# Performance work log

Measured on AMD Instinct MI355X. Metric: run time of the kernel, lower is better.

The kernel has to match this reference:

```python
import jax, jax.numpy as jnp
import numpy as np

HIDDEN = 50
EPS = 1e-5


def setup_inputs() -> dict:
    key = jax.random.key(0)
    ks = jax.random.split(key, 16)
    N = 1_000_000
    G = 10_000
    xy = jax.random.normal(ks[0], (N, 2), dtype=jnp.float32)
    segment_ids = jnp.sort(jax.random.randint(ks[1], (N,), 0, G, dtype=jnp.int32))

    def lin(k, fan_in, shape):
        b = 1.0 / np.sqrt(fan_in)
        return jax.random.uniform(k, shape, jnp.float32, -b, b)

    w_init = lin(ks[2], 2, (2, HIDDEN))
    b_init = lin(ks[3], 2, (HIDDEN,))
    Ws1 = lin(ks[4], 2 * HIDDEN, (2, 2 * HIDDEN, HIDDEN))
    bs1 = lin(ks[5], 2 * HIDDEN, (2, HIDDEN))
    Ws = lin(ks[6], HIDDEN, (2, 4, HIDDEN, HIDDEN))
    bs = lin(ks[7], HIDDEN, (2, 4, HIDDEN))
    gamma = jnp.ones((2, HIDDEN), jnp.float32)
    beta = jnp.zeros((2, HIDDEN), jnp.float32)
    return {
        'xy': xy, 'segment_ids': segment_ids, 'num_graphs': G,
        'w_init': w_init, 'b_init': b_init,
        'Ws1': Ws1, 'bs1': bs1, 'Ws': Ws, 'bs': bs,
        'gamma': gamma, 'beta': beta,
    }


def reference(xy, segment_ids, num_graphs, w_init, b_init, Ws1, bs1, Ws, bs, gamma, beta):
    # node_init: [N,2] -> [N,50]
    h = xy @ w_init + b_init
    ones = jnp.ones((xy.shape[0],), h.dtype)
    counts = jax.ops.segment_sum(ones, segment_ids, num_segments=num_graphs)
    counts = jnp.maximum(counts, 1.0)[:, None]  # [G,1]
    for i in range(2):
        # dgl.mean_nodes -> per-graph mean; dgl.broadcast_nodes -> gather back
        mean = jax.ops.segment_sum(h, segment_ids, num_segments=num_graphs) / counts
        glob = mean[segment_ids]                       # [N,50]
        x = jnp.concatenate([glob, h], axis=1)         # [N,100]
        x = jax.nn.relu(x @ Ws1[i] + bs1[i])
        for j in range(3):
            x = jax.nn.relu(x @ Ws[i, j] + bs[i, j])
        x = x @ Ws[i, 3] + bs[i, 3]
        # BatchNorm1d (training mode: batch stats, biased variance)
        mu = jnp.mean(x, axis=0)
        var = jnp.mean((x - mu) ** 2, axis=0)
        h = (x - mu) * jax.lax.rsqrt(var + EPS) * gamma[i] + beta[i]
    return h
```

## Files before the change

kernel.cpp:

```cpp
#include <hip/hip_runtime.h>


#define GN 10000
#define H 50
#define EPSV 1e-5f

typedef __attribute__((ext_vector_type(4))) float f32x4;
typedef __attribute__((ext_vector_type(2))) __fp16 fp16x2;
typedef __attribute__((ext_vector_type(4))) _Float16 half4_t;

union H4 { half4_t h; uint2 u; };

static __device__ __forceinline__ f32x4 mfma16(half4_t a, half4_t b, f32x4 c){
#if __has_builtin(__builtin_amdgcn_mfma_f32_16x16x16f16)
  return __builtin_amdgcn_mfma_f32_16x16x16f16(a, b, c, 0, 0, 0);
#else
  asm volatile("v_mfma_f32_16x16x16_f16 %0, %1, %2, %0" : "+v"(c) : "v"(a), "v"(b));
  return c;
#endif
}

static __device__ __forceinline__ void split4(f32x4 v, H4& hh, H4& hl){
  fp16x2 a = __builtin_amdgcn_cvt_pkrtz(v[0], v[1]);
  fp16x2 b = __builtin_amdgcn_cvt_pkrtz(v[2], v[3]);
  hh.u.x = __builtin_bit_cast(unsigned int, a);
  hh.u.y = __builtin_bit_cast(unsigned int, b);
  float r0 = v[0] - (float)a[0];
  float r1 = v[1] - (float)a[1];
  float r2 = v[2] - (float)b[0];
  float r3 = v[3] - (float)b[1];
  fp16x2 c = __builtin_amdgcn_cvt_pkrtz(r0, r1);
  fp16x2 d = __builtin_amdgcn_cvt_pkrtz(r2, r3);
  hl.u.x = __builtin_bit_cast(unsigned int, c);
  hl.u.y = __builtin_bit_cast(unsigned int, d);
}

__global__ void k_start(const int* __restrict__ sid, int N, int* __restrict__ start){
  int g = blockIdx.x*blockDim.x + threadIdx.x;
  if (g > GN) return;
  int lo = 0, hi = N;
  while (lo < hi){ int mid = (lo+hi)>>1; if (sid[mid] < g) lo = mid+1; else hi = mid; }
  start[g] = lo;
}

__global__ void k_gsum_xy(const float2* __restrict__ xy, const int* __restrict__ start,
                          float* __restrict__ gxy){
  int g = blockIdx.x; int l = threadIdx.x;
  int s = start[g], e = start[g+1];
  float sx = 0.f, sy = 0.f;
  for (int n = s + l; n < e; n += 64){ float2 v = xy[n]; sx += v.x; sy += v.y; }
  #pragma unroll
  for (int off = 32; off > 0; off >>= 1){ sx += __shfl_down(sx, off); sy += __shfl_down(sy, off); }
  if (l == 0){ gxy[2*g] = sx; gxy[2*g+1] = sy; }
}

template<int LAYER>
__global__ void k_tgraph(const float* __restrict__ gxy, const float* __restrict__ gsum,
                         const int* __restrict__ start,
                         const float* __restrict__ w_init, const float* __restrict__ b_init,
                         const float* __restrict__ Ws1, const float* __restrict__ bs1,
                         const float* __restrict__ stats, float* __restrict__ tg){
  __shared__ float glob[H];
  int g = blockIdx.x; int j = threadIdx.x;
  int cnt = start[g+1] - start[g]; if (cnt < 1) cnt = 1;
  float inv = 1.f/(float)cnt;
  if (j < H){
    if (LAYER == 0){
      float mx = gxy[2*g]*inv, my = gxy[2*g+1]*inv;
      glob[j] = b_init[j] + mx*w_init[j] + my*w_init[H+j];
    } else {
      glob[j] = gsum[g*H+j]*inv*stats[j] + stats[H+j];
    }
  }
  __syncthreads();
  if (j < H){
    const float* W = Ws1 + LAYER*100*H;
    float acc = bs1[LAYER*H + j];
    #pragma unroll 5
    for (int k = 0; k < H; ++k) acc = fmaf(glob[k], W[k*H + j], acc);
    tg[g*H + j] = acc;
  }
}

__global__ void k_wfrag(const float* __restrict__ Ws1, const float* __restrict__ Ws,
                        const float* __restrict__ bs,
                        uint2* __restrict__ frag, float* __restrict__ pbias){
  int t = blockIdx.x*blockDim.x + threadIdx.x;
  if (t < 20480){
    int lane = t & 63;
    int pl   = (t>>6) & 1;
    int ks   = (t>>7) & 3;
    int Mt   = (t>>9) & 3;
    int rest = t >> 11;
    int m = rest % 5, L = rest / 5;
    const float* W = (m == 0) ? (Ws1 + L*100*H + H*H) : (Ws + (L*4 + (m-1))*H*H);
    int jo = Mt*16 + (lane & 15);
    int kb = ks*16 + ((lane>>4)<<2);
    f32x4 v;
    #pragma unroll
    for (int e = 0; e < 4; ++e){
      int k = kb + e;
      v[e] = (k < H && jo < H) ? W[k*H + jo] : 0.f;
    }
    H4 hh, hl;
    split4(v, hh, hl);
    frag[t] = pl ? hl.u : hh.u;
  } else if (t < 20992){
    int i = t - 20480;
    int j = i & 63;
    int row = i >> 6;
    pbias[i] = (j < H) ? bs[row*H + j] : 0.f;
  }
}

template<int LAYER>
__global__ __launch_bounds__(256, 3)
void k_layer(const float2* __restrict__ xy, const int* __restrict__ sid,
             const float* __restrict__ tg, const uint2* __restrict__ frag,
             const float* __restrict__ pbias,
             const float* __restrict__ w_init, const float* __restrict__ b_init,
             const float* __restrict__ stats,
             float* __restrict__ xio, int N)
{
  const int tid = threadIdx.x;
  const int wv = tid >> 6, l = tid & 63, lg = l >> 4, ll = l & 15;
  const int base = blockIdx.x*128 + wv*32;

  H4 bh[2][4], bl[2][4];
  #pragma unroll
  for (int Nt = 0; Nt < 2; ++Nt){
    int node = base + Nt*16 + ll;
    int nc = node < N ? node : N-1;
    float xv[16];
    if (LAYER == 0){
      float2 p = xy[nc];
      #pragma unroll
      for (int ks = 0; ks < 4; ++ks)
        #pragma unroll
        for (int e = 0; e < 4; ++e){
          int k = ks*16 + lg*4 + e; int kc = k < H ? k : H-1;
          xv[ks*4+e] = b_init[kc] + p.x*w_init[kc] + p.y*w_init[H+kc];
        }
    } else {
      #pragma unroll
      for (int ks = 0; ks < 4; ++ks){
        int k0 = ks*16 + lg*4;
        size_t f0 = (size_t)nc*H + k0;
        size_t fm = (size_t)N*H - 2;
        float2 u0 = *(const float2*)(xio + (f0     < fm ? f0     : fm));
        float2 u1 = *(const float2*)(xio + (f0 + 2 < fm ? f0 + 2 : fm));
        float vv[4] = {u0.x, u0.y, u1.x, u1.y};
        #pragma unroll
        for (int e = 0; e < 4; ++e){
          int kc = (k0+e) < H ? (k0+e) : H-1;
          xv[ks*4+e] = vv[e]*stats[kc] + stats[H+kc];
        }
      }
    }
    #pragma unroll
    for (int ks = 0; ks < 4; ++ks){
      f32x4 v; v[0]=xv[ks*4]; v[1]=xv[ks*4+1]; v[2]=xv[ks*4+2]; v[3]=xv[ks*4+3];
      split4(v, bh[Nt][ks], bl[Nt][ks]);
    }
  }

  f32x4 acc[4][2];
  {
    int n0 = base + ll;       n0 = n0 < N ? n0 : N-1;
    int n1 = base + 16 + ll;  n1 = n1 < N ? n1 : N-1;
    const float* t0 = tg + (size_t)sid[n0]*H;
    const float* t1 = tg + (size_t)sid[n1]*H;
    #pragma unroll
    for (int Mt = 0; Mt < 4; ++Mt)
      #pragma unroll
      for (int r = 0; r < 4; ++r){
        int j = Mt*16 + lg*4 + r; int jc = j < H ? j : H-1;
        acc[Mt][0][r] = t0[jc];
        acc[Mt][1][r] = t1[jc];
      }
  }

  #pragma unroll
  for (int m = 0; m < 5; ++m){
    const uint2* fp = frag + (LAYER*5 + m)*2048;
    #pragma unroll
    for (int Mt = 0; Mt < 4; ++Mt){
      H4 ah[4], al[4];
      #pragma unroll
      for (int ks = 0; ks < 4; ++ks){
        ah[ks].u = fp[Mt*512 + ks*128 + l];
        al[ks].u = fp[Mt*512 + ks*128 + 64 + l];
      }
      #pragma unroll
      for (int Nt = 0; Nt < 2; ++Nt){
        f32x4 c = acc[Mt][Nt];
        #pragma unroll
        for (int ks = 0; ks < 4; ++ks) c = mfma16(ah[ks].h, bh[Nt][ks].h, c);
        #pragma unroll
        for (int ks = 0; ks < 4; ++ks) c = mfma16(al[ks].h, bh[Nt][ks].h, c);
        #pragma unroll
        for (int ks = 0; ks < 4; ++ks) c = mfma16(ah[ks].h, bl[Nt][ks].h, c);
        acc[Mt][Nt] = c;
      }
    }
    if (m < 4){
      #pragma unroll
      for (int Mt = 0; Mt < 4; ++Mt){
        const f32x4 bv = *(const f32x4*)(pbias + (LAYER*4 + m)*64 + Mt*16 + (lg<<2));
        #pragma unroll
        for (int Nt = 0; Nt < 2; ++Nt){
          f32x4 v = acc[Mt][Nt];
          v[0]=fmaxf(v[0],0.f); v[1]=fmaxf(v[1],0.f); v[2]=fmaxf(v[2],0.f); v[3]=fmaxf(v[3],0.f);
          split4(v, bh[Nt][Mt], bl[Nt][Mt]);
          acc[Mt][Nt] = bv;
        }
      }
    }
  }

  #pragma unroll
  for (int Nt = 0; Nt < 2; ++Nt){
    int node = base + Nt*16 + ll;
    if (node < N){
      float* row = xio + (size_t)node*H;
      #pragma unroll
      for (int Mt = 0; Mt < 3; ++Mt){
        int j0 = Mt*16 + (lg<<2);
        *(float2*)(row + j0)     = make_float2(acc[Mt][Nt][0], acc[Mt][Nt][1]);
        *(float2*)(row + j0 + 2) = make_float2(acc[Mt][Nt][2], acc[Mt][Nt][3]);
      }
      if (lg == 0)
        *(float2*)(row + 48) = make_float2(acc[3][Nt][0], acc[3][Nt][1]);
    }
  }
}

__global__ void k_stats(const float* __restrict__ x, const int* __restrict__ start,
                        float* __restrict__ gsum, float* __restrict__ psum,
                        float* __restrict__ psq){
  int g = blockIdx.x; int j = threadIdx.x;
  if (j >= H) return;
  int s = start[g], e = start[g+1];
  float acc = 0.f, q = 0.f;
  for (int n = s; n < e; ++n){ float v = x[n*H + j]; acc += v; q = fmaf(v, v, q); }
  gsum[g*H + j] = acc;
  int slot = g & 63;
  atomicAdd(&psum[slot*H + j], acc);
  atomicAdd(&psq[slot*H + j], q);
}

__global__ void k_finalize(const float* __restrict__ psum, const float* __restrict__ psq,
                           const float* __restrict__ gamma, const float* __restrict__ beta,
                           int layer, float ninv, float* __restrict__ stats){
  int j = threadIdx.x;
  if (j >= H) return;
  float s = 0.f, q = 0.f;
  #pragma unroll 8
  for (int p = 0; p < 64; ++p){ s += psum[p*H + j]; q += psq[p*H + j]; }
  float mu  = s*ninv;
  float var = q*ninv - mu*mu;
  float a = rsqrtf(var + EPSV) * gamma[layer*H + j];
  float c = beta[layer*H + j] - mu*a;
  stats[layer*100 + j]     = a;
  stats[layer*100 + H + j] = c;
}

__global__ void k_bnapply(float* __restrict__ x, const float* __restrict__ stats, int N){
  __shared__ float a[H], c[H];
  if (threadIdx.x < H){ a[threadIdx.x] = stats[100 + threadIdx.x]; c[threadIdx.x] = stats[150 + threadIdx.x]; }
  __syncthreads();
  int base = blockIdx.x * (256*H);
  int total = N*H;
  for (int idx = threadIdx.x; idx < 256*H; idx += 256){
    int i = base + idx;
    if (i < total){
      int j = idx - (idx/H)*H;
      x[i] = x[i]*a[j] + c[j];
    }
  }
}

extern "C" void kernel_launch(void* const* d_in, const int* in_sizes, int n_in,
                              void* d_out, int out_size, void* d_ws, size_t ws_size,
                              hipStream_t stream) {
  const float2* xy     = (const float2*)d_in[0];
  const int*    sid    = (const int*)d_in[1];
  const float*  w_init = (const float*)d_in[3];
  const float*  b_init = (const float*)d_in[4];
  const float*  Ws1    = (const float*)d_in[5];
  const float*  bs1    = (const float*)d_in[6];
  const float*  Ws     = (const float*)d_in[7];
  const float*  bs     = (const float*)d_in[8];
  const float*  gamma  = (const float*)d_in[9];
  const float*  beta   = (const float*)d_in[10];
  float* out = (float*)d_out;
  int N = in_sizes[0] / 2;
  const int G = GN;

  char* ws = (char*)d_ws;
  int*   start = (int*)ws;
  float* gxy   = (float*)(ws + 40064);
  float* tg    = (float*)(ws + 120064);
  float* gsum  = (float*)(ws + 2120064);
  float* psum  = (float*)(ws + 4120064);
  float* psq   = (float*)(ws + 4132864);
  float* stats = (float*)(ws + 4145664);
  uint2* wfrag = (uint2*)(ws + 4147200);
  float* pbias = (float*)(ws + 4311040);

  int nb = (N + 127)/128;

  k_wfrag<<<82, 256, 0, stream>>>(Ws1, Ws, bs, wfrag, pbias);
  k_start<<<(G + 1 + 255)/256, 256, 0, stream>>>(sid, N, start);
  k_gsum_xy<<<G, 64, 0, stream>>>(xy, start, gxy);
  k_tgraph<0><<<G, 64, 0, stream>>>(gxy, gsum, start, w_init, b_init, Ws1, bs1, stats, tg);
  k_layer<0><<<nb, 256, 0, stream>>>(xy, sid, tg, wfrag, pbias, w_init, b_init, stats, out, N);

  (void)hipMemsetAsync(psum, 0, 2*64*H*sizeof(float), stream);
  k_stats<<<G, 64, 0, stream>>>(out, start, gsum, psum, psq);
  k_finalize<<<1, 64, 0, stream>>>(psum, psq, gamma, beta, 0, 1.0f/(float)N, stats);

  k_tgraph<1><<<G, 64, 0, stream>>>(gxy, gsum, start, w_init, b_init, Ws1, bs1, stats, tg);
  k_layer<1><<<nb, 256, 0, stream>>>(xy, sid, tg, wfrag, pbias, w_init, b_init, stats, out, N);

  (void)hipMemsetAsync(psum, 0, 2*64*H*sizeof(float), stream);
  k_stats<<<G, 64, 0, stream>>>(out, start, gsum, psum, psq);
  k_finalize<<<1, 64, 0, stream>>>(psum, psq, gamma, beta, 1, 1.0f/(float)N, stats);

  k_bnapply<<<(N + 255)/256, 256, 0, stream>>>(out, stats, N);
}
```

Measured before the change: 839.5 us.

## Fuse BN statistics into layer kernel and merge setup kernels

Each MFMA layer kernel now reduces per-feature sum and sum-of-squares from its register accumulators and atomically adds them into slot buffers, which removes the separate per-graph stats pass over the 200MB activation. The graph-sum for layer 1 moves into a new kernel that also computes the transformed global term. Weight fragment prep, segment-start search and the psum zeroing are merged into one pre-kernel, and k_finalize re-zeroes the buffers so the memsets go away. Weight fragments are packed as uint4 so the hi and lo halves load together. The cost is atomic traffic from every block and an extra activation read in k_gt1.

```diff
diff --git a/kernel.cpp b/kernel.cpp
--- a/kernel.cpp
+++ b/kernel.cpp
@@ -35,91 +35,75 @@
   hl.u.y = __builtin_bit_cast(unsigned int, d);
 }
 
-__global__ void k_start(const int* __restrict__ sid, int N, int* __restrict__ start){
-  int g = blockIdx.x*blockDim.x + threadIdx.x;
-  if (g > GN) return;
-  int lo = 0, hi = N;
-  while (lo < hi){ int mid = (lo+hi)>>1; if (sid[mid] < g) lo = mid+1; else hi = mid; }
-  start[g] = lo;
-}
-
-__global__ void k_gsum_xy(const float2* __restrict__ xy, const int* __restrict__ start,
-                          float* __restrict__ gxy){
+__global__ void k_pre(const float* __restrict__ Ws1, const float* __restrict__ Ws,
+                      const float* __restrict__ bs, const int* __restrict__ sid, int N,
+                      uint4* __restrict__ frag, float* __restrict__ pbias,
+                      int* __restrict__ start, float* __restrict__ pzero){
+  int t = blockIdx.x*blockDim.x + threadIdx.x;
+  if (t < 10240){
+    int lane = t & 63;
+    int ks   = (t>>6) & 3;
+    int Mt   = (t>>8) & 3;
+    int rest = t >> 10;
+    int m = rest % 5, L = rest / 5;
+    const float* W = (m == 0) ? (Ws1 + L*100*H + H*H) : (Ws + (L*4 + (m-1))*H*H);
+    int jo = Mt*16 + (lane & 15);
+    int kb = ks*16 + ((lane>>4)<<2);
+    f32x4 v;
+    #pragma unroll
+    for (int e = 0; e < 4; ++e){
+      int k = kb + e;
+      v[e] = (k < H && jo < H) ? W[k*H + jo] : 0.f;
+    }
+    H4 hh, hl;
+    split4(v, hh, hl);
+    frag[t] = make_uint4(hh.u.x, hh.u.y, hl.u.x, hl.u.y);
+  } else if (t < 10752){
+    int i = t - 10240;
+    int j = i & 63;
+    int row = i >> 6;
+    pbias[i] = (j < H) ? bs[row*H + j] : 0.f;
+  } else if (t < 20753){
+    int g = t - 10752;
+    int lo = 0, hi = N;
+    while (lo < hi){ int mid = (lo+hi)>>1; if (sid[mid] < g) lo = mid+1; else hi = mid; }
+    start[g] = lo;
+  } else if (t >= 20800 && t < 27200){
+    pzero[t - 20800] = 0.f;
+  }
+}
+
+__global__ void k_ginit0(const float2* __restrict__ xy, const int* __restrict__ start,
+                         const float* __restrict__ w_init, const float* __restrict__ b_init,
+                         const float* __restrict__ Ws1, const float* __restrict__ bs1,
+                         float* __restrict__ tg){
+  __shared__ float glob[H];
   int g = blockIdx.x; int l = threadIdx.x;
   int s = start[g], e = start[g+1];
   float sx = 0.f, sy = 0.f;
   for (int n = s + l; n < e; n += 64){ float2 v = xy[n]; sx += v.x; sy += v.y; }
   #pragma unroll
-  for (int off = 32; off > 0; off >>= 1){ sx += __shfl_down(sx, off); sy += __shfl_down(sy, off); }
-  if (l == 0){ gxy[2*g] = sx; gxy[2*g+1] = sy; }
-}
-
-template<int LAYER>
-__global__ void k_tgraph(const float* __restrict__ gxy, const float* __restrict__ gsum,
-                         const int* __restrict__ start,
-                         const float* __restrict__ w_init, const float* __restrict__ b_init,
-                         const float* __restrict__ Ws1, const float* __restrict__ bs1,
-                         const float* __restrict__ stats, float* __restrict__ tg){
-  __shared__ float glob[H];
-  int g = blockIdx.x; int j = threadIdx.x;
-  int cnt = start[g+1] - start[g]; if (cnt < 1) cnt = 1;
+  for (int off = 32; off > 0; off >>= 1){ sx += __shfl_xor(sx, off); sy += __shfl_xor(sy, off); }
+  int cnt = e - s; if (cnt < 1) cnt = 1;
   float inv = 1.f/(float)cnt;
-  if (j < H){
-    if (LAYER == 0){
-      float mx = gxy[2*g]*inv, my = gxy[2*g+1]*inv;
-      glob[j] = b_init[j] + mx*w_init[j] + my*w_init[H+j];
-    } else {
-      glob[j] = gsum[g*H+j]*inv*stats[j] + stats[H+j];
-    }
-  }
+  if (l < H) glob[l] = b_init[l] + sx*inv*w_init[l] + sy*inv*w_init[H+l];
   __syncthreads();
-  if (j < H){
-    const float* W = Ws1 + LAYER*100*H;
-    float acc = bs1[LAYER*H + j];
+  if (l < H){
+    float a = bs1[l];
     #pragma unroll 5
-    for (int k = 0; k < H; ++k) acc = fmaf(glob[k], W[k*H + j], acc);
-    tg[g*H + j] = acc;
-  }
-}
-
-__global__ void k_wfrag(const float* __restrict__ Ws1, const float* __restrict__ Ws,
-                        const float* __restrict__ bs,
-                        uint2* __restrict__ frag, float* __restrict__ pbias){
-  int t = blockIdx.x*blockDim.x + threadIdx.x;
-  if (t < 20480){
-    int lane = t & 63;
-    int pl   = (t>>6) & 1;
-    int ks   = (t>>7) & 3;
-    int Mt   = (t>>9) & 3;
-    int rest = t >> 11;
-    int m = rest % 5, L = rest / 5;
-    const float* W = (m == 0) ? (Ws1 + L*100*H + H*H) : (Ws + (L*4 + (m-1))*H*H);
-    int jo = Mt*16 + (lane & 15);
-    int kb = ks*16 + ((lane>>4)<<2);
-    f32x4 v;
-    #pragma unroll
-    for (int e = 0; e < 4; ++e){
-      int k = kb + e;
-      v[e] = (k < H && jo < H) ? W[k*H + jo] : 0.f;
-    }
-    H4 hh, hl;
-    split4(v, hh, hl);
-    frag[t] = pl ? hl.u : hh.u;
-  } else if (t < 20992){
-    int i = t - 20480;
-    int j = i & 63;
-    int row = i >> 6;
-    pbias[i] = (j < H) ? bs[row*H + j] : 0.f;
+    for (int k = 0; k < H; ++k) a = fmaf(glob[k], Ws1[k*H + l], a);
+    tg[(size_t)g*H + l] = a;
   }
 }
 
 template<int LAYER>
 __global__ __launch_bounds__(256, 3)
 void k_layer(const float2* __restrict__ xy, const int* __restrict__ sid,
-             const float* __restrict__ tg, const uint2* __restrict__ frag,
+             const float* __restrict__ tg, const uint4* __restrict__ frag,
              const float* __restrict__ pbias,
              const float* __restrict__ w_init, const float* __restrict__ b_init,
              const float* __restrict__ stats,
+             float* __restrict__ psum, float* __restrict__ psq,
              float* __restrict__ xio, int N)
 {
   const int tid = threadIdx.x;
@@ -182,14 +166,15 @@
 
   #pragma unroll
   for (int m = 0; m < 5; ++m){
-    const uint2* fp = frag + (LAYER*5 + m)*2048;
+    const uint4* fp = frag + (LAYER*5 + m)*1024;
     #pragma unroll
     for (int Mt = 0; Mt < 4; ++Mt){
       H4 ah[4], al[4];
       #pragma unroll
       for (int ks = 0; ks < 4; ++ks){
-        ah[ks].u = fp[Mt*512 + ks*128 + l];
-        al[ks].u = fp[Mt*512 + ks*128 + 64 + l];
+        uint4 w = fp[(Mt*4 + ks)*64 + l];
+        ah[ks].u = make_uint2(w.x, w.y);
+        al[ks].u = make_uint2(w.z, w.w);
       }
       #pragma unroll
       for (int Nt = 0; Nt < 2; ++Nt){
@@ -233,23 +218,32 @@
         *(float2*)(row + 48) = make_float2(acc[3][Nt][0], acc[3][Nt][1]);
     }
   }
-}
-
-__global__ void k_stats(const float* __restrict__ x, const int* __restrict__ start,
-                        float* __restrict__ gsum, float* __restrict__ psum,
-                        float* __restrict__ psq){
-  int g = blockIdx.x; int j = threadIdx.x;
-  if (j >= H) return;
-  int s = start[g], e = start[g+1];
-  float acc = 0.f, q = 0.f;
-  for (int n = s; n < e; ++n){ float v = x[n*H + j]; acc += v; q = fmaf(v, v, q); }
-  gsum[g*H + j] = acc;
-  int slot = g & 63;
-  atomicAdd(&psum[slot*H + j], acc);
-  atomicAdd(&psq[slot*H + j], q);
-}
-
-__global__ void k_finalize(const float* __restrict__ psum, const float* __restrict__ psq,
+
+  {
+    int slot = (int)(blockIdx.x & 63);
+    #pragma unroll
+    for (int Mt = 0; Mt < 4; ++Mt)
+      #pragma unroll
+      for (int r = 0; r < 4; ++r){
+        int j = Mt*16 + lg*4 + r;
+        float s = 0.f, q = 0.f;
+        #pragma unroll
+        for (int Nt = 0; Nt < 2; ++Nt){
+          int node = base + Nt*16 + ll;
+          float v = (node < N && j < H) ? acc[Mt][Nt][r] : 0.f;
+          s += v; q = fmaf(v, v, q);
+        }
+        #pragma unroll
+        for (int off = 8; off > 0; off >>= 1){ s += __shfl_xor(s, off); q += __shfl_xor(q, off); }
+        if (ll == 0 && j < H){
+          atomicAdd(&psum[slot*H + j], s);
+          atomicAdd(&psq [slot*H + j], q);
+        }
+      }
+  }
+}
+
+__global__ void k_finalize(float* __restrict__ psum, float* __restrict__ psq,
                            const float* __restrict__ gamma, const float* __restrict__ beta,
                            int layer, float ninv, float* __restrict__ stats){
   int j = threadIdx.x;
@@ -263,6 +257,32 @@
   float c = beta[layer*H + j] - mu*a;
   stats[layer*100 + j]     = a;
   stats[layer*100 + H + j] = c;
+  #pragma unroll 8
+  for (int p = 0; p < 64; ++p){ psum[p*H + j] = 0.f; psq[p*H + j] = 0.f; }
+}
+
+__global__ void k_gt1(const float* __restrict__ x, const int* __restrict__ start,
+                      const float* __restrict__ stats,
+                      const float* __restrict__ Ws1, const float* __restrict__ bs1,
+                      float* __restrict__ tg){
+  __shared__ float glob[H];
+  int g = blockIdx.x; int j = threadIdx.x;
+  int s = start[g], e = start[g+1];
+  int cnt = e - s; if (cnt < 1) cnt = 1;
+  float inv = 1.f/(float)cnt;
+  if (j < H){
+    float acc = 0.f;
+    for (int n = s; n < e; ++n) acc += x[(size_t)n*H + j];
+    glob[j] = acc*inv*stats[j] + stats[H+j];
+  }
+  __syncthreads();
+  if (j < H){
+    const float* W = Ws1 + 100*H;
+    float a = bs1[H + j];
+    #pragma unroll 5
+    for (int k = 0; k < H; ++k) a = fmaf(glob[k], W[k*H + j], a);
+    tg[(size_t)g*H + j] = a;
+  }
 }
 
 __global__ void k_bnapply(float* __restrict__ x, const float* __restrict__ stats, int N){
@@ -299,33 +319,21 @@
 
   char* ws = (char*)d_ws;
   int*   start = (int*)ws;
-  float* gxy   = (float*)(ws + 40064);
-  float* tg    = (float*)(ws + 120064);
-  float* gsum  = (float*)(ws + 2120064);
-  float* psum  = (float*)(ws + 4120064);
-  float* psq   = (float*)(ws + 4132864);
-  float* stats = (float*)(ws + 4145664);
-  uint2* wfrag = (uint2*)(ws + 4147200);
-  float* pbias = (float*)(ws + 4311040);
+  float* tg    = (float*)(ws + 40064);
+  float* psum  = (float*)(ws + 2040064);
+  float* psq   = (float*)(ws + 2052864);
+  float* stats = (float*)(ws + 2065664);
+  uint4* frag  = (uint4*)(ws + 2066560);
+  float* pbias = (float*)(ws + 2230400);
 
   int nb = (N + 127)/128;
 
-  k_wfrag<<<82, 256, 0, stream>>>(Ws1, Ws, bs, wfrag, pbias);
-  k_start<<<(G + 1 + 255)/256, 256, 0, stream>>>(sid, N, start);
-  k_gsum_xy<<<G, 64, 0, stream>>>(xy, start, gxy);
-  k_tgraph<0><<<G, 64, 0, stream>>>(gxy, gsum, start, w_init, b_init, Ws1, bs1, stats, tg);
-  k_layer<0><<<nb, 256, 0, stream>>>(xy, sid, tg, wfrag, pbias, w_init, b_init, stats, out, N);
-
-  (void)hipMemsetAsync(psum, 0, 2*64*H*sizeof(float), stream);
-  k_stats<<<G, 64, 0, stream>>>(out, start, gsum, psum, psq);
+  k_pre<<<107, 256, 0, stream>>>(Ws1, Ws, bs, sid, N, frag, pbias, start, psum);
+  k_ginit0<<<G, 64, 0, stream>>>(xy, start, w_init, b_init, Ws1, bs1, tg);
+  k_layer<0><<<nb, 256, 0, stream>>>(xy, sid, tg, frag, pbias, w_init, b_init, stats, psum, psq, out, N);
   k_finalize<<<1, 64, 0, stream>>>(psum, psq, gamma, beta, 0, 1.0f/(float)N, stats);
-
-  k_tgraph<1><<<G, 64, 0, stream>>>(gxy, gsum, start, w_init, b_init, Ws1, bs1, stats, tg);
-  k_layer<1><<<nb, 256, 0, stream>>>(xy, sid, tg, wfrag, pbias, w_init, b_init, stats, out, N);
-
-  (void)hipMemsetAsync(psum, 0, 2*64*H*sizeof(float), stream);
-  k_stats<<<G, 64, 0, stream>>>(out, start, gsum, psum, psq);
+  k_gt1<<<G, 64, 0, stream>>>(out, start, stats, Ws1, bs1, tg);
+  k_layer<1><<<nb, 256, 0, stream>>>(xy, sid, tg, frag, pbias, w_init, b_init, stats, psum, psq, out, N);
   k_finalize<<<1, 64, 0, stream>>>(psum, psq, gamma, beta, 1, 1.0f/(float)N, stats);
-
   k_bnapply<<<(N + 255)/256, 256, 0, stream>>>(out, stats, N);
 }
```

Measured after the change: 731.0 us. 12.9% less time.
